# Kernel optimization log

Measured on AMD Instinct MI355X. Metric: run time of the kernel, lower is better.

## Reference

```python
import jax, jax.numpy as jnp
import numpy as np

B, H, S, D = 4, 16, 2048, 64  # head_dim = num_dims // num_heads = 1024 // 16


def setup_inputs() -> dict:
    key = jax.random.key(0)
    kq, kk, kv = jax.random.split(key, 3)
    q = jax.random.normal(kq, (B, H, S, D), dtype=jnp.float32)
    k = jax.random.normal(kk, (B, H, S, D), dtype=jnp.float32)
    v = jax.random.normal(kv, (B, H, S, D), dtype=jnp.float32)
    return {"q": q, "k": k, "v": v}


def reference(q, k, v):
    # scores = (q @ k^T) / sqrt(head_dim)  -> [B, H, S, S]
    scale = 1.0 / np.sqrt(D).astype(np.float32)
    scores = jnp.einsum("bhqd,bhkd->bhqk", q, k) * scale
    # softmax over keys; dropout rate is 0.0 (eval), so it's the identity
    weights = jax.nn.softmax(scores, axis=-1)
    # weights @ v -> [B, H, S, D]
    return jnp.einsum("bhqk,bhkd->bhqd", weights, v)
```

## Files before the change

### kernel.cpp

```cpp
#include <hip/hip_runtime.h>
#include <hip/hip_bf16.h>

#define S_LEN 2048
#define BH_TOTAL 64
#define D_DIM 64
#define NT 32

typedef float f32x4 __attribute__((ext_vector_type(4)));
typedef float f32x16 __attribute__((ext_vector_type(16)));
typedef __bf16 bf16x8 __attribute__((ext_vector_type(8)));
typedef unsigned short u16x8 __attribute__((ext_vector_type(8)));
typedef unsigned int u32;
typedef u32 u32x2 __attribute__((ext_vector_type(2)));
typedef u32 u32x4 __attribute__((ext_vector_type(4)));

union BF8 { u32x4 w; u16x8 u; bf16x8 b; };

#if __has_builtin(__builtin_amdgcn_exp2f)
#define EX2(x) __builtin_amdgcn_exp2f(x)
#else
#define EX2(x) exp2f(x)
#endif

__device__ __forceinline__ unsigned short f2b(float f) {
  __bf16 h = (__bf16)f;
  return __builtin_bit_cast(unsigned short, h);
}
__device__ __forceinline__ u32 pk2(float a, float b) {
  return (u32)f2b(a) | ((u32)f2b(b) << 16);
}

__device__ __forceinline__ u32x2 pl32(u32 x, u32 y) {
#if __has_builtin(__builtin_amdgcn_permlane32_swap)
  return __builtin_amdgcn_permlane32_swap(x, y, false, false);
#else
  u32 xs = (u32)__shfl_xor((int)x, 32);
  u32 ys = (u32)__shfl_xor((int)y, 32);
  int hi = (int)(threadIdx.x & 32);
  u32x2 r;
  r.x = hi ? ys : x;
  r.y = hi ? y : xs;
  return r;
#endif
}

__device__ __forceinline__ void gload16(const unsigned short* g, unsigned short* l) {
  __builtin_amdgcn_global_load_lds(
      (const __attribute__((address_space(1))) unsigned int*)g,
      (__attribute__((address_space(3))) unsigned int*)l, 16, 0, 0);
}

__global__ __launch_bounds__(256)
void cvt_k(const float* __restrict__ K, unsigned short* __restrict__ Kb) {
  int i = blockIdx.x * 256 + threadIdx.x;
  const f32x4* src = (const f32x4*)K;
  f32x4 a = src[2 * i], b = src[2 * i + 1];
  u16x8 o;
  #pragma unroll
  for (int j = 0; j < 4; ++j) { o[j] = f2b(a[j]); o[j + 4] = f2b(b[j]); }
  ((u16x8*)Kb)[i] = o;
}

__global__ __launch_bounds__(256)
void tr_v(const float* __restrict__ V, unsigned short* __restrict__ Vt) {
  __shared__ unsigned short T[64][72];
  int bh = blockIdx.x >> 5, t5 = blockIdx.x & 31;
  int s0 = t5 * 64;
  int tid = threadIdx.x;
  {
    int s = tid >> 2, d0 = (tid & 3) * 16;
    const float* src = V + ((size_t)bh * S_LEN + s0 + s) * D_DIM + d0;
    #pragma unroll
    for (int j = 0; j < 16; j += 4) {
      f32x4 x = *(const f32x4*)(src + j);
      #pragma unroll
      for (int q2 = 0; q2 < 4; ++q2) T[d0 + j + q2][s] = f2b(x[q2]);
    }
  }
  __syncthreads();
  {
    int d = tid >> 2, c0 = (tid & 3) * 16;
    unsigned short* dst = Vt + ((size_t)bh * D_DIM + d) * S_LEN + s0 + c0;
    u16x8 o;
    #pragma unroll
    for (int q2 = 0; q2 < 8; ++q2) o[q2] = T[d][c0 + q2];
    *(u16x8*)dst = o;
    #pragma unroll
    for (int q2 = 0; q2 < 8; ++q2) o[q2] = T[d][c0 + 8 + q2];
    *(u16x8*)(dst + 8) = o;
  }
}

__device__ __forceinline__ void exppack(const f32x16 sv, float& ls, BF8& pA, BF8& pB) {
  u32 wlo[4], whi[4];
  #pragma unroll
  for (int b2 = 0; b2 < 4; ++b2) {
    float e0 = EX2(sv[4 * b2 + 0]), e1 = EX2(sv[4 * b2 + 1]);
    float e2 = EX2(sv[4 * b2 + 2]), e3 = EX2(sv[4 * b2 + 3]);
    ls += (e0 + e1) + (e2 + e3);
    wlo[b2] = pk2(e0, e1);
    whi[b2] = pk2(e2, e3);
  }
  u32x2 rlo = pl32(wlo[0], wlo[1]);
  u32x2 rhi = pl32(whi[0], whi[1]);
  pA.w[0] = rlo.x; pA.w[1] = rhi.x; pA.w[2] = rlo.y; pA.w[3] = rhi.y;
  rlo = pl32(wlo[2], wlo[3]);
  rhi = pl32(whi[2], whi[3]);
  pB.w[0] = rlo.x; pB.w[1] = rhi.x; pB.w[2] = rlo.y; pB.w[3] = rhi.y;
}

#define MFMA32(A, B, C) __builtin_amdgcn_mfma_f32_32x32x16_bf16((A), (B), (C), 0, 0, 0)

__global__ __launch_bounds__(256, 4)
void attn_fwd(const float* __restrict__ Q, const unsigned short* __restrict__ Kb,
              const unsigned short* __restrict__ Vt, float* __restrict__ O) {
  const int wg = blockIdx.x;
  const int id = (wg & 7) * 128 + (wg >> 3);
  const int qt = id & 15;
  const int bh = id >> 4;

  const int tid = threadIdx.x;
  const int w = tid >> 6;
  const int ln = tid & 63;
  const int l31 = ln & 31;
  const int h = ln >> 5;

  __shared__ __align__(16) unsigned short Ks[2][4096];
  __shared__ __align__(16) unsigned short Vs[2][4096];

  const size_t hbase = (size_t)bh * S_LEN * D_DIM;
  const unsigned short* Kh = Kb + hbase;
  const unsigned short* Vh = Vt + hbase;

  const int q0 = qt * 128 + w * 32;

  BF8 qf[4];
  {
    const float sc = 0.125f * 1.44269504088896f;
    const float* qp = Q + hbase + (size_t)(q0 + l31) * D_DIM + h * 8;
    #pragma unroll
    for (int f = 0; f < 4; ++f) {
      f32x4 a = *(const f32x4*)(qp + f * 16);
      f32x4 b = *(const f32x4*)(qp + f * 16 + 4);
      #pragma unroll
      for (int j = 0; j < 4; ++j) {
        qf[f].u[j]     = f2b(a[j] * sc);
        qf[f].u[j + 4] = f2b(b[j] * sc);
      }
    }
  }

  const int srow = ln >> 3;
  const int scol = ((ln & 7) ^ srow) * 8;
  const unsigned short* ks0 = Kh + (size_t)(w * 16 + srow) * D_DIM + scol;
  const unsigned short* vs0 = Vh + (size_t)(w * 16 + srow) * S_LEN + scol;

  const int swz = (ln & 7) << 4;
  const int rb = l31 * 128;
  int cx[4];
  #pragma unroll
  for (int m = 0; m < 4; ++m) cx[m] = (m * 32 + h * 16) ^ swz;

  f32x16 oa0, oa1, zc;
  #pragma unroll
  for (int j = 0; j < 16; ++j) { oa0[j] = 0.f; oa1[j] = 0.f; zc[j] = 0.f; }
  float ls = 0.f;

  gload16(ks0,             &Ks[0][w * 1024]);
  gload16(ks0 + 512,       &Ks[0][w * 1024 + 512]);
  gload16(vs0,             &Vs[0][w * 1024]);
  gload16(vs0 + 8 * S_LEN, &Vs[0][w * 1024 + 512]);
  __syncthreads();

  for (int t = 0; t < NT; ++t) {
    const int cur = t & 1;
    if (t + 1 < NT) {
      const unsigned short* kp = ks0 + (size_t)(t + 1) * 4096;
      const unsigned short* vp = vs0 + (t + 1) * 64;
      gload16(kp,             &Ks[cur ^ 1][w * 1024]);
      gload16(kp + 512,       &Ks[cur ^ 1][w * 1024 + 512]);
      gload16(vp,             &Vs[cur ^ 1][w * 1024]);
      gload16(vp + 8 * S_LEN, &Vs[cur ^ 1][w * 1024 + 512]);
    }

    const char* KsB = (const char*)&Ks[cur][0];
    const char* VsB = (const char*)&Vs[cur][0];

    BF8 ka, kb, kc, kd;
    ka.u = *(const u16x8*)(KsB + rb + cx[0]);
    kb.u = *(const u16x8*)(KsB + 4096 + rb + cx[0]);
    kc.u = *(const u16x8*)(KsB + rb + cx[1]);
    kd.u = *(const u16x8*)(KsB + 4096 + rb + cx[1]);
    f32x16 s0, s1;
    __builtin_amdgcn_s_setprio(1);
    s0 = MFMA32(ka.b, qf[0].b, zc);
    s1 = MFMA32(kb.b, qf[0].b, zc);
    ka.u = *(const u16x8*)(KsB + rb + cx[2]);
    kb.u = *(const u16x8*)(KsB + 4096 + rb + cx[2]);
    s0 = MFMA32(kc.b, qf[1].b, s0);
    s1 = MFMA32(kd.b, qf[1].b, s1);
    kc.u = *(const u16x8*)(KsB + rb + cx[3]);
    kd.u = *(const u16x8*)(KsB + 4096 + rb + cx[3]);
    s0 = MFMA32(ka.b, qf[2].b, s0);
    s1 = MFMA32(kb.b, qf[2].b, s1);
    s0 = MFMA32(kc.b, qf[3].b, s0);
    s1 = MFMA32(kd.b, qf[3].b, s1);
    __builtin_amdgcn_s_setprio(0);

    BF8 va, vb, vc, vd;
    va.u = *(const u16x8*)(VsB + rb + cx[0]);
    vb.u = *(const u16x8*)(VsB + 4096 + rb + cx[0]);
    vc.u = *(const u16x8*)(VsB + rb + cx[1]);
    vd.u = *(const u16x8*)(VsB + 4096 + rb + cx[1]);

    BF8 pf0, pf1, pf2, pf3;
    exppack(s0, ls, pf0, pf1);
    exppack(s1, ls, pf2, pf3);

    __builtin_amdgcn_s_setprio(1);
    oa0 = MFMA32(va.b, pf0.b, oa0);
    oa1 = MFMA32(vb.b, pf0.b, oa1);
    va.u = *(const u16x8*)(VsB + rb + cx[2]);
    vb.u = *(const u16x8*)(VsB + 4096 + rb + cx[2]);
    oa0 = MFMA32(vc.b, pf1.b, oa0);
    oa1 = MFMA32(vd.b, pf1.b, oa1);
    vc.u = *(const u16x8*)(VsB + rb + cx[3]);
    vd.u = *(const u16x8*)(VsB + 4096 + rb + cx[3]);
    oa0 = MFMA32(va.b, pf2.b, oa0);
    oa1 = MFMA32(vb.b, pf2.b, oa1);
    oa0 = MFMA32(vc.b, pf3.b, oa0);
    oa1 = MFMA32(vd.b, pf3.b, oa1);
    __builtin_amdgcn_s_setprio(0);

    __syncthreads();
  }

  {
    float lo2 = __shfl_xor(ls, 32);
    float inv = 1.0f / (ls + lo2);
    float* op = O + hbase + (size_t)(q0 + l31) * D_DIM;
    #pragma unroll
    for (int dt = 0; dt < 2; ++dt) {
      const f32x16 oa = dt ? oa1 : oa0;
      #pragma unroll
      for (int b2 = 0; b2 < 4; ++b2) {
        f32x4 vv;
        vv[0] = oa[4 * b2 + 0] * inv;
        vv[1] = oa[4 * b2 + 1] * inv;
        vv[2] = oa[4 * b2 + 2] * inv;
        vv[3] = oa[4 * b2 + 3] * inv;
        *(f32x4*)(op + dt * 32 + b2 * 8 + h * 4) = vv;
      }
    }
  }
}

extern "C" void kernel_launch(void* const* d_in, const int* in_sizes, int n_in,
                              void* d_out, int out_size, void* d_ws, size_t ws_size,
                              hipStream_t stream) {
  const float* q = (const float*)d_in[0];
  const float* k = (const float*)d_in[1];
  const float* v = (const float*)d_in[2];
  float* o = (float*)d_out;
  unsigned short* kb = (unsigned short*)d_ws;
  unsigned short* vt = kb + (size_t)BH_TOTAL * S_LEN * D_DIM;

  cvt_k<<<dim3(4096), 256, 0, stream>>>(k, kb);
  tr_v<<<dim3(2048), 256, 0, stream>>>(v, vt);
  attn_fwd<<<dim3(1024), 256, 0, stream>>>(q, kb, vt, o);
}
```

Before: 112.3 us.

## Triple-buffer K/V LDS tiles with two-deep prefetch and partial vmcnt waits

Switches the K/V shared-memory staging from double to triple buffering, prefetching two tiles ahead with rotating buffer pointers. The full __syncthreads is replaced by s_waitcnt vmcnt(4) plus s_barrier, so only the older tile's loads must finish before each iteration. This hides more global-load latency, but LDS use rises from 32KB to 48KB per block and the launch-bounds occupancy hint drops from 4 to 3 blocks. The zero accumulators for S are now reinitialised inside the loop.

```diff
diff --git a/kernel.cpp b/kernel.cpp
--- a/kernel.cpp
+++ b/kernel.cpp
@@ -111,7 +111,7 @@
 
 #define MFMA32(A, B, C) __builtin_amdgcn_mfma_f32_32x32x16_bf16((A), (B), (C), 0, 0, 0)
 
-__global__ __launch_bounds__(256, 4)
+__global__ __launch_bounds__(256, 3)
 void attn_fwd(const float* __restrict__ Q, const unsigned short* __restrict__ Kb,
               const unsigned short* __restrict__ Vt, float* __restrict__ O) {
   const int wg = blockIdx.x;
@@ -125,8 +125,8 @@
   const int l31 = ln & 31;
   const int h = ln >> 5;
 
-  __shared__ __align__(16) unsigned short Ks[2][4096];
-  __shared__ __align__(16) unsigned short Vs[2][4096];
+  __shared__ __align__(16) unsigned short Ks[3][4096];
+  __shared__ __align__(16) unsigned short Vs[3][4096];
 
   const size_t hbase = (size_t)bh * S_LEN * D_DIM;
   const unsigned short* Kh = Kb + hbase;
@@ -161,46 +161,56 @@
   #pragma unroll
   for (int m = 0; m < 4; ++m) cx[m] = (m * 32 + h * 16) ^ swz;
 
-  f32x16 oa0, oa1, zc;
-  #pragma unroll
-  for (int j = 0; j < 16; ++j) { oa0[j] = 0.f; oa1[j] = 0.f; zc[j] = 0.f; }
+  f32x16 oa0, oa1;
+  #pragma unroll
+  for (int j = 0; j < 16; ++j) { oa0[j] = 0.f; oa1[j] = 0.f; }
   float ls = 0.f;
 
-  gload16(ks0,             &Ks[0][w * 1024]);
-  gload16(ks0 + 512,       &Ks[0][w * 1024 + 512]);
-  gload16(vs0,             &Vs[0][w * 1024]);
-  gload16(vs0 + 8 * S_LEN, &Vs[0][w * 1024 + 512]);
-  __syncthreads();
+  gload16(ks0,                  &Ks[0][w * 1024]);
+  gload16(ks0 + 512,            &Ks[0][w * 1024 + 512]);
+  gload16(vs0,                  &Vs[0][w * 1024]);
+  gload16(vs0 + 8 * S_LEN,      &Vs[0][w * 1024 + 512]);
+  gload16(ks0 + 4096,           &Ks[1][w * 1024]);
+  gload16(ks0 + 4096 + 512,     &Ks[1][w * 1024 + 512]);
+  gload16(vs0 + 64,             &Vs[1][w * 1024]);
+  gload16(vs0 + 64 + 8 * S_LEN, &Vs[1][w * 1024 + 512]);
+  asm volatile("s_waitcnt vmcnt(4)" ::: "memory");
+  __builtin_amdgcn_s_barrier();
+
+  const char* kA = (const char*)&Ks[0][0];
+  const char* kB = (const char*)&Ks[1][0];
+  char*       kC = (char*)&Ks[2][0];
+  const char* vA = (const char*)&Vs[0][0];
+  const char* vB = (const char*)&Vs[1][0];
+  char*       vC = (char*)&Vs[2][0];
 
   for (int t = 0; t < NT; ++t) {
-    const int cur = t & 1;
-    if (t + 1 < NT) {
-      const unsigned short* kp = ks0 + (size_t)(t + 1) * 4096;
-      const unsigned short* vp = vs0 + (t + 1) * 64;
-      gload16(kp,             &Ks[cur ^ 1][w * 1024]);
-      gload16(kp + 512,       &Ks[cur ^ 1][w * 1024 + 512]);
-      gload16(vp,             &Vs[cur ^ 1][w * 1024]);
-      gload16(vp + 8 * S_LEN, &Vs[cur ^ 1][w * 1024 + 512]);
-    }
-
-    const char* KsB = (const char*)&Ks[cur][0];
-    const char* VsB = (const char*)&Vs[cur][0];
+    if (t + 2 < NT) {
+      const unsigned short* kp = ks0 + (size_t)(t + 2) * 4096;
+      const unsigned short* vp = vs0 + (t + 2) * 64;
+      gload16(kp,             (unsigned short*)kC + w * 1024);
+      gload16(kp + 512,       (unsigned short*)kC + w * 1024 + 512);
+      gload16(vp,             (unsigned short*)vC + w * 1024);
+      gload16(vp + 8 * S_LEN, (unsigned short*)vC + w * 1024 + 512);
+    }
 
     BF8 ka, kb, kc, kd;
-    ka.u = *(const u16x8*)(KsB + rb + cx[0]);
-    kb.u = *(const u16x8*)(KsB + 4096 + rb + cx[0]);
-    kc.u = *(const u16x8*)(KsB + rb + cx[1]);
-    kd.u = *(const u16x8*)(KsB + 4096 + rb + cx[1]);
+    ka.u = *(const u16x8*)(kA + rb + cx[0]);
+    kb.u = *(const u16x8*)(kA + 4096 + rb + cx[0]);
+    kc.u = *(const u16x8*)(kA + rb + cx[1]);
+    kd.u = *(const u16x8*)(kA + 4096 + rb + cx[1]);
     f32x16 s0, s1;
+    #pragma unroll
+    for (int j = 0; j < 16; ++j) { s0[j] = 0.f; s1[j] = 0.f; }
     __builtin_amdgcn_s_setprio(1);
-    s0 = MFMA32(ka.b, qf[0].b, zc);
-    s1 = MFMA32(kb.b, qf[0].b, zc);
-    ka.u = *(const u16x8*)(KsB + rb + cx[2]);
-    kb.u = *(const u16x8*)(KsB + 4096 + rb + cx[2]);
+    s0 = MFMA32(ka.b, qf[0].b, s0);
+    s1 = MFMA32(kb.b, qf[0].b, s1);
+    ka.u = *(const u16x8*)(kA + rb + cx[2]);
+    kb.u = *(const u16x8*)(kA + 4096 + rb + cx[2]);
     s0 = MFMA32(kc.b, qf[1].b, s0);
     s1 = MFMA32(kd.b, qf[1].b, s1);
-    kc.u = *(const u16x8*)(KsB + rb + cx[3]);
-    kd.u = *(const u16x8*)(KsB + 4096 + rb + cx[3]);
+    kc.u = *(const u16x8*)(kA + rb + cx[3]);
+    kd.u = *(const u16x8*)(kA + 4096 + rb + cx[3]);
     s0 = MFMA32(ka.b, qf[2].b, s0);
     s1 = MFMA32(kb.b, qf[2].b, s1);
     s0 = MFMA32(kc.b, qf[3].b, s0);
@@ -208,10 +218,10 @@
     __builtin_amdgcn_s_setprio(0);
 
     BF8 va, vb, vc, vd;
-    va.u = *(const u16x8*)(VsB + rb + cx[0]);
-    vb.u = *(const u16x8*)(VsB + 4096 + rb + cx[0]);
-    vc.u = *(const u16x8*)(VsB + rb + cx[1]);
-    vd.u = *(const u16x8*)(VsB + 4096 + rb + cx[1]);
+    va.u = *(const u16x8*)(vA + rb + cx[0]);
+    vb.u = *(const u16x8*)(vA + 4096 + rb + cx[0]);
+    vc.u = *(const u16x8*)(vA + rb + cx[1]);
+    vd.u = *(const u16x8*)(vA + 4096 + rb + cx[1]);
 
     BF8 pf0, pf1, pf2, pf3;
     exppack(s0, ls, pf0, pf1);
@@ -220,19 +230,27 @@
     __builtin_amdgcn_s_setprio(1);
     oa0 = MFMA32(va.b, pf0.b, oa0);
     oa1 = MFMA32(vb.b, pf0.b, oa1);
-    va.u = *(const u16x8*)(VsB + rb + cx[2]);
-    vb.u = *(const u16x8*)(VsB + 4096 + rb + cx[2]);
+    va.u = *(const u16x8*)(vA + rb + cx[2]);
+    vb.u = *(const u16x8*)(vA + 4096 + rb + cx[2]);
     oa0 = MFMA32(vc.b, pf1.b, oa0);
     oa1 = MFMA32(vd.b, pf1.b, oa1);
-    vc.u = *(const u16x8*)(VsB + rb + cx[3]);
-    vd.u = *(const u16x8*)(VsB + 4096 + rb + cx[3]);
+    vc.u = *(const u16x8*)(vA + rb + cx[3]);
+    vd.u = *(const u16x8*)(vA + 4096 + rb + cx[3]);
     oa0 = MFMA32(va.b, pf2.b, oa0);
     oa1 = MFMA32(vb.b, pf2.b, oa1);
     oa0 = MFMA32(vc.b, pf3.b, oa0);
     oa1 = MFMA32(vd.b, pf3.b, oa1);
     __builtin_amdgcn_s_setprio(0);
 
-    __syncthreads();
+    if (t + 2 < NT) {
+      asm volatile("s_waitcnt vmcnt(4)" ::: "memory");
+    } else {
+      asm volatile("s_waitcnt vmcnt(0)" ::: "memory");
+    }
+    __builtin_amdgcn_s_barrier();
+
+    { const char* tmp = kA; kA = kB; kB = (const char*)kC; kC = (char*)tmp; }
+    { const char* tmp = vA; vA = vB; vB = (const char*)vC; vC = (char*)tmp; }
   }
 
   {
```

Result: slower. 116.0 us (+3.3%).

## Restructure attention K/V pipeline with per-wave full-tile loads and vmcnt waits

Applied to the files above, without the earlier changes.

The attention main loop is rewritten so each wave issues global-to-LDS loads for the whole next K/V tile itself. Synchronisation now uses explicit vmcnt waits plus a raw s_barrier in place of __syncthreads. The score computation is split into two 32-key halves, each followed by its exp/pack and P·V MFMAs, to interleave work and shrink live registers. The K conversion and V transpose prep kernels are merged into one launch. In exchange, every wave fetches the full tile, so global and L2 load traffic is four times larger, and the hand-written wait counts depend on how the compiler orders the loads.

```diff
diff --git a/kernel.cpp b/kernel.cpp
--- a/kernel.cpp
+++ b/kernel.cpp
@@ -51,43 +51,44 @@
 }
 
 __global__ __launch_bounds__(256)
-void cvt_k(const float* __restrict__ K, unsigned short* __restrict__ Kb) {
-  int i = blockIdx.x * 256 + threadIdx.x;
-  const f32x4* src = (const f32x4*)K;
-  f32x4 a = src[2 * i], b = src[2 * i + 1];
-  u16x8 o;
-  #pragma unroll
-  for (int j = 0; j < 4; ++j) { o[j] = f2b(a[j]); o[j + 4] = f2b(b[j]); }
-  ((u16x8*)Kb)[i] = o;
-}
-
-__global__ __launch_bounds__(256)
-void tr_v(const float* __restrict__ V, unsigned short* __restrict__ Vt) {
+void prep(const float* __restrict__ K, const float* __restrict__ V,
+          unsigned short* __restrict__ Kb, unsigned short* __restrict__ Vt) {
   __shared__ unsigned short T[64][72];
-  int bh = blockIdx.x >> 5, t5 = blockIdx.x & 31;
-  int s0 = t5 * 64;
-  int tid = threadIdx.x;
-  {
-    int s = tid >> 2, d0 = (tid & 3) * 16;
-    const float* src = V + ((size_t)bh * S_LEN + s0 + s) * D_DIM + d0;
-    #pragma unroll
-    for (int j = 0; j < 16; j += 4) {
-      f32x4 x = *(const f32x4*)(src + j);
-      #pragma unroll
-      for (int q2 = 0; q2 < 4; ++q2) T[d0 + j + q2][s] = f2b(x[q2]);
-    }
-  }
-  __syncthreads();
-  {
-    int d = tid >> 2, c0 = (tid & 3) * 16;
-    unsigned short* dst = Vt + ((size_t)bh * D_DIM + d) * S_LEN + s0 + c0;
+  if (blockIdx.x < 4096) {
+    int i = blockIdx.x * 256 + threadIdx.x;
+    const f32x4* src = (const f32x4*)K;
+    f32x4 a = src[2 * i], b = src[2 * i + 1];
     u16x8 o;
     #pragma unroll
-    for (int q2 = 0; q2 < 8; ++q2) o[q2] = T[d][c0 + q2];
-    *(u16x8*)dst = o;
-    #pragma unroll
-    for (int q2 = 0; q2 < 8; ++q2) o[q2] = T[d][c0 + 8 + q2];
-    *(u16x8*)(dst + 8) = o;
+    for (int j = 0; j < 4; ++j) { o[j] = f2b(a[j]); o[j + 4] = f2b(b[j]); }
+    ((u16x8*)Kb)[i] = o;
+  } else {
+    int bid = blockIdx.x - 4096;
+    int bh = bid >> 5, t5 = bid & 31;
+    int s0 = t5 * 64;
+    int tid = threadIdx.x;
+    {
+      int s = tid >> 2, d0 = (tid & 3) * 16;
+      const float* src = V + ((size_t)bh * S_LEN + s0 + s) * D_DIM + d0;
+      #pragma unroll
+      for (int j = 0; j < 16; j += 4) {
+        f32x4 x = *(const f32x4*)(src + j);
+        #pragma unroll
+        for (int q2 = 0; q2 < 4; ++q2) T[d0 + j + q2][s] = f2b(x[q2]);
+      }
+    }
+    __syncthreads();
+    {
+      int d = tid >> 2, c0 = (tid & 3) * 16;
+      unsigned short* dst = Vt + ((size_t)bh * D_DIM + d) * S_LEN + s0 + c0;
+      u16x8 o;
+      #pragma unroll
+      for (int q2 = 0; q2 < 8; ++q2) o[q2] = T[d][c0 + q2];
+      *(u16x8*)dst = o;
+      #pragma unroll
+      for (int q2 = 0; q2 < 8; ++q2) o[q2] = T[d][c0 + 8 + q2];
+      *(u16x8*)(dst + 8) = o;
+    }
   }
 }
 
@@ -111,6 +112,67 @@
 
 #define MFMA32(A, B, C) __builtin_amdgcn_mfma_f32_32x32x16_bf16((A), (B), (C), 0, 0, 0)
 
+#define STAGE(tt, SB) do {                                                   \
+    const unsigned short* kp_ = kbase + (size_t)(tt) * 4096;                 \
+    const unsigned short* vp_ = vbase + (tt) * 64;                           \
+    gload16(kp_ + 0 * 512, &Ks[SB][0 * 512]);                                \
+    gload16(kp_ + 1 * 512, &Ks[SB][1 * 512]);                                \
+    gload16(kp_ + 2 * 512, &Ks[SB][2 * 512]);                                \
+    gload16(kp_ + 3 * 512, &Ks[SB][3 * 512]);                                \
+    gload16(kp_ + 4 * 512, &Ks[SB][4 * 512]);                                \
+    gload16(kp_ + 5 * 512, &Ks[SB][5 * 512]);                                \
+    gload16(kp_ + 6 * 512, &Ks[SB][6 * 512]);                                \
+    gload16(kp_ + 7 * 512, &Ks[SB][7 * 512]);                                \
+    gload16(vp_ + (size_t)0 * 8 * S_LEN, &Vs[SB][0 * 512]);                  \
+    gload16(vp_ + (size_t)1 * 8 * S_LEN, &Vs[SB][1 * 512]);                  \
+    gload16(vp_ + (size_t)2 * 8 * S_LEN, &Vs[SB][2 * 512]);                  \
+    gload16(vp_ + (size_t)3 * 8 * S_LEN, &Vs[SB][3 * 512]);                  \
+    gload16(vp_ + (size_t)4 * 8 * S_LEN, &Vs[SB][4 * 512]);                  \
+    gload16(vp_ + (size_t)5 * 8 * S_LEN, &Vs[SB][5 * 512]);                  \
+    gload16(vp_ + (size_t)6 * 8 * S_LEN, &Vs[SB][6 * 512]);                  \
+    gload16(vp_ + (size_t)7 * 8 * S_LEN, &Vs[SB][7 * 512]);                  \
+  } while (0)
+
+#define ITER(tt, RB, SB, DOSTAGE) do {                                       \
+    if (DOSTAGE) { STAGE((tt) + 1, SB); }                                    \
+    const char* KsB_ = (const char*)&Ks[RB][0];                              \
+    const char* VsB_ = (const char*)&Vs[RB][0];                              \
+    _Pragma("unroll")                                                        \
+    for (int kt = 0; kt < 2; ++kt) {                                         \
+      BF8 k0_, k1_, k2_, k3_;                                                \
+      k0_.u = *(const u16x8*)(KsB_ + kt * 4096 + rb + cx[0]);                \
+      k1_.u = *(const u16x8*)(KsB_ + kt * 4096 + rb + cx[1]);                \
+      k2_.u = *(const u16x8*)(KsB_ + kt * 4096 + rb + cx[2]);                \
+      k3_.u = *(const u16x8*)(KsB_ + kt * 4096 + rb + cx[3]);                \
+      f32x16 s_;                                                             \
+      _Pragma("unroll")                                                      \
+      for (int j = 0; j < 16; ++j) s_[j] = 0.f;                              \
+      __builtin_amdgcn_s_setprio(1);                                         \
+      s_ = MFMA32(k0_.b, qf[0].b, s_);                                       \
+      s_ = MFMA32(k1_.b, qf[1].b, s_);                                       \
+      s_ = MFMA32(k2_.b, qf[2].b, s_);                                       \
+      s_ = MFMA32(k3_.b, qf[3].b, s_);                                       \
+      __builtin_amdgcn_s_setprio(0);                                         \
+      BF8 pA_, pB_;                                                          \
+      exppack(s_, ls, pA_, pB_);                                             \
+      if (kt == 0) {                                                         \
+        if (DOSTAGE) asm volatile("s_waitcnt vmcnt(16)" ::: "memory");       \
+        else         asm volatile("s_waitcnt vmcnt(0)"  ::: "memory");       \
+      }                                                                      \
+      BF8 vA0_, vA1_, vB0_, vB1_;                                            \
+      vA0_.u = *(const u16x8*)(VsB_ + rb + cx[2 * kt]);                      \
+      vA1_.u = *(const u16x8*)(VsB_ + 4096 + rb + cx[2 * kt]);               \
+      vB0_.u = *(const u16x8*)(VsB_ + rb + cx[2 * kt + 1]);                  \
+      vB1_.u = *(const u16x8*)(VsB_ + 4096 + rb + cx[2 * kt + 1]);           \
+      __builtin_amdgcn_s_setprio(1);                                         \
+      oa0 = MFMA32(vA0_.b, pA_.b, oa0);                                      \
+      oa1 = MFMA32(vA1_.b, pA_.b, oa1);                                      \
+      oa0 = MFMA32(vB0_.b, pB_.b, oa0);                                      \
+      oa1 = MFMA32(vB1_.b, pB_.b, oa1);                                      \
+      __builtin_amdgcn_s_setprio(0);                                         \
+    }                                                                        \
+  } while (0)
+
 __global__ __launch_bounds__(256, 4)
 void attn_fwd(const float* __restrict__ Q, const unsigned short* __restrict__ Kb,
               const unsigned short* __restrict__ Vt, float* __restrict__ O) {
@@ -152,8 +214,8 @@
 
   const int srow = ln >> 3;
   const int scol = ((ln & 7) ^ srow) * 8;
-  const unsigned short* ks0 = Kh + (size_t)(w * 16 + srow) * D_DIM + scol;
-  const unsigned short* vs0 = Vh + (size_t)(w * 16 + srow) * S_LEN + scol;
+  const unsigned short* kbase = Kh + srow * D_DIM + scol;
+  const unsigned short* vbase = Vh + (size_t)srow * S_LEN + scol;
 
   const int swz = (ln & 7) << 4;
   const int rb = l31 * 128;
@@ -161,79 +223,27 @@
   #pragma unroll
   for (int m = 0; m < 4; ++m) cx[m] = (m * 32 + h * 16) ^ swz;
 
-  f32x16 oa0, oa1, zc;
+  f32x16 oa0, oa1;
   #pragma unroll
-  for (int j = 0; j < 16; ++j) { oa0[j] = 0.f; oa1[j] = 0.f; zc[j] = 0.f; }
+  for (int j = 0; j < 16; ++j) { oa0[j] = 0.f; oa1[j] = 0.f; }
   float ls = 0.f;
 
-  gload16(ks0,             &Ks[0][w * 1024]);
-  gload16(ks0 + 512,       &Ks[0][w * 1024 + 512]);
-  gload16(vs0,             &Vs[0][w * 1024]);
-  gload16(vs0 + 8 * S_LEN, &Vs[0][w * 1024 + 512]);
-  __syncthreads();
-
-  for (int t = 0; t < NT; ++t) {
-    const int cur = t & 1;
-    if (t + 1 < NT) {
-      const unsigned short* kp = ks0 + (size_t)(t + 1) * 4096;
-      const unsigned short* vp = vs0 + (t + 1) * 64;
-      gload16(kp,             &Ks[cur ^ 1][w * 1024]);
-      gload16(kp + 512,       &Ks[cur ^ 1][w * 1024 + 512]);
-      gload16(vp,             &Vs[cur ^ 1][w * 1024]);
-      gload16(vp + 8 * S_LEN, &Vs[cur ^ 1][w * 1024 + 512]);
-    }
-
-    const char* KsB = (const char*)&Ks[cur][0];
-    const char* VsB = (const char*)&Vs[cur][0];
-
-    BF8 ka, kb, kc, kd;
-    ka.u = *(const u16x8*)(KsB + rb + cx[0]);
-    kb.u = *(const u16x8*)(KsB + 4096 + rb + cx[0]);
-    kc.u = *(const u16x8*)(KsB + rb + cx[1]);
-    kd.u = *(const u16x8*)(KsB + 4096 + rb + cx[1]);
-    f32x16 s0, s1;
-    __builtin_amdgcn_s_setprio(1);
-    s0 = MFMA32(ka.b, qf[0].b, zc);
-    s1 = MFMA32(kb.b, qf[0].b, zc);
-    ka.u = *(const u16x8*)(KsB + rb + cx[2]);
-    kb.u = *(const u16x8*)(KsB + 4096 + rb + cx[2]);
-    s0 = MFMA32(kc.b, qf[1].b, s0);
-    s1 = MFMA32(kd.b, qf[1].b, s1);
-    kc.u = *(const u16x8*)(KsB + rb + cx[3]);
-    kd.u = *(const u16x8*)(KsB + 4096 + rb + cx[3]);
-    s0 = MFMA32(ka.b, qf[2].b, s0);
-    s1 = MFMA32(kb.b, qf[2].b, s1);
-    s0 = MFMA32(kc.b, qf[3].b, s0);
-    s1 = MFMA32(kd.b, qf[3].b, s1);
-    __builtin_amdgcn_s_setprio(0);
-
-    BF8 va, vb, vc, vd;
-    va.u = *(const u16x8*)(VsB + rb + cx[0]);
-    vb.u = *(const u16x8*)(VsB + 4096 + rb + cx[0]);
-    vc.u = *(const u16x8*)(VsB + rb + cx[1]);
-    vd.u = *(const u16x8*)(VsB + 4096 + rb + cx[1]);
-
-    BF8 pf0, pf1, pf2, pf3;
-    exppack(s0, ls, pf0, pf1);
-    exppack(s1, ls, pf2, pf3);
-
-    __builtin_amdgcn_s_setprio(1);
-    oa0 = MFMA32(va.b, pf0.b, oa0);
-    oa1 = MFMA32(vb.b, pf0.b, oa1);
-    va.u = *(const u16x8*)(VsB + rb + cx[2]);
-    vb.u = *(const u16x8*)(VsB + 4096 + rb + cx[2]);
-    oa0 = MFMA32(vc.b, pf1.b, oa0);
-    oa1 = MFMA32(vd.b, pf1.b, oa1);
-    vc.u = *(const u16x8*)(VsB + rb + cx[3]);
-    vd.u = *(const u16x8*)(VsB + 4096 + rb + cx[3]);
-    oa0 = MFMA32(va.b, pf2.b, oa0);
-    oa1 = MFMA32(vb.b, pf2.b, oa1);
-    oa0 = MFMA32(vc.b, pf3.b, oa0);
-    oa1 = MFMA32(vd.b, pf3.b, oa1);
-    __builtin_amdgcn_s_setprio(0);
-
-    __syncthreads();
-  }
+  STAGE(0, 0);
+  asm volatile("s_waitcnt vmcnt(8)" ::: "memory");
+  __builtin_amdgcn_s_barrier();
+
+  for (int t2 = 0; t2 < NT - 2; t2 += 2) {
+    ITER(t2, 0, 1, 1);
+    asm volatile("s_waitcnt vmcnt(8)" ::: "memory");
+    __builtin_amdgcn_s_barrier();
+    ITER(t2 + 1, 1, 0, 1);
+    asm volatile("s_waitcnt vmcnt(8)" ::: "memory");
+    __builtin_amdgcn_s_barrier();
+  }
+  ITER(NT - 2, 0, 1, 1);
+  asm volatile("s_waitcnt vmcnt(8)" ::: "memory");
+  __builtin_amdgcn_s_barrier();
+  ITER(NT - 1, 1, 0, 0);
 
   {
     float lo2 = __shfl_xor(ls, 32);
@@ -265,7 +275,6 @@
   unsigned short* kb = (unsigned short*)d_ws;
   unsigned short* vt = kb + (size_t)BH_TOTAL * S_LEN * D_DIM;
 
-  cvt_k<<<dim3(4096), 256, 0, stream>>>(k, kb);
-  tr_v<<<dim3(2048), 256, 0, stream>>>(v, vt);
+  prep<<<dim3(4096 + 2048), 256, 0, stream>>>(k, v, kb, vt);
   attn_fwd<<<dim3(1024), 256, 0, stream>>>(q, kb, vt, o);
 }
```

New measurement: 144.4 us. +28.6%, slower.

## Enlarge attention workgroups to 8 waves with 128-key tiles and fuse prep kernels

Applied to the files above, without the earlier changes.

The attention kernel now uses 512-thread workgroups covering 256 queries. Each loop iteration stages 128 keys as two 64-key chunks, which halves the number of barriers and makes each staged K/V tile serve twice as many queries. The K conversion and V transpose kernels are merged into one launch, saving a kernel launch. The risk is that `__launch_bounds__(512, 4)` implies 8 waves per SIMD, which could cap registers low enough to cause spills given the large MFMA accumulator state.

```diff
diff --git a/kernel.cpp b/kernel.cpp
--- a/kernel.cpp
+++ b/kernel.cpp
@@ -4,7 +4,7 @@
 #define S_LEN 2048
 #define BH_TOTAL 64
 #define D_DIM 64
-#define NT 32
+#define NT2 16
 
 typedef float f32x4 __attribute__((ext_vector_type(4)));
 typedef float f32x16 __attribute__((ext_vector_type(16)));
@@ -51,43 +51,44 @@
 }
 
 __global__ __launch_bounds__(256)
-void cvt_k(const float* __restrict__ K, unsigned short* __restrict__ Kb) {
-  int i = blockIdx.x * 256 + threadIdx.x;
-  const f32x4* src = (const f32x4*)K;
-  f32x4 a = src[2 * i], b = src[2 * i + 1];
-  u16x8 o;
-  #pragma unroll
-  for (int j = 0; j < 4; ++j) { o[j] = f2b(a[j]); o[j + 4] = f2b(b[j]); }
-  ((u16x8*)Kb)[i] = o;
-}
-
-__global__ __launch_bounds__(256)
-void tr_v(const float* __restrict__ V, unsigned short* __restrict__ Vt) {
+void prep(const float* __restrict__ K, const float* __restrict__ V,
+          unsigned short* __restrict__ Kb, unsigned short* __restrict__ Vt) {
   __shared__ unsigned short T[64][72];
-  int bh = blockIdx.x >> 5, t5 = blockIdx.x & 31;
-  int s0 = t5 * 64;
-  int tid = threadIdx.x;
-  {
-    int s = tid >> 2, d0 = (tid & 3) * 16;
-    const float* src = V + ((size_t)bh * S_LEN + s0 + s) * D_DIM + d0;
-    #pragma unroll
-    for (int j = 0; j < 16; j += 4) {
-      f32x4 x = *(const f32x4*)(src + j);
-      #pragma unroll
-      for (int q2 = 0; q2 < 4; ++q2) T[d0 + j + q2][s] = f2b(x[q2]);
-    }
-  }
-  __syncthreads();
-  {
-    int d = tid >> 2, c0 = (tid & 3) * 16;
-    unsigned short* dst = Vt + ((size_t)bh * D_DIM + d) * S_LEN + s0 + c0;
+  if (blockIdx.x < 4096) {
+    int i = blockIdx.x * 256 + threadIdx.x;
+    const f32x4* src = (const f32x4*)K;
+    f32x4 a = src[2 * i], b = src[2 * i + 1];
     u16x8 o;
     #pragma unroll
-    for (int q2 = 0; q2 < 8; ++q2) o[q2] = T[d][c0 + q2];
-    *(u16x8*)dst = o;
-    #pragma unroll
-    for (int q2 = 0; q2 < 8; ++q2) o[q2] = T[d][c0 + 8 + q2];
-    *(u16x8*)(dst + 8) = o;
+    for (int j = 0; j < 4; ++j) { o[j] = f2b(a[j]); o[j + 4] = f2b(b[j]); }
+    ((u16x8*)Kb)[i] = o;
+  } else {
+    int bid = blockIdx.x - 4096;
+    int bh = bid >> 5, t5 = bid & 31;
+    int s0 = t5 * 64;
+    int tid = threadIdx.x;
+    {
+      int s = tid >> 2, d0 = (tid & 3) * 16;
+      const float* src = V + ((size_t)bh * S_LEN + s0 + s) * D_DIM + d0;
+      #pragma unroll
+      for (int j = 0; j < 16; j += 4) {
+        f32x4 x = *(const f32x4*)(src + j);
+        #pragma unroll
+        for (int q2 = 0; q2 < 4; ++q2) T[d0 + j + q2][s] = f2b(x[q2]);
+      }
+    }
+    __syncthreads();
+    {
+      int d = tid >> 2, c0 = (tid & 3) * 16;
+      unsigned short* dst = Vt + ((size_t)bh * D_DIM + d) * S_LEN + s0 + c0;
+      u16x8 o;
+      #pragma unroll
+      for (int q2 = 0; q2 < 8; ++q2) o[q2] = T[d][c0 + q2];
+      *(u16x8*)dst = o;
+      #pragma unroll
+      for (int q2 = 0; q2 < 8; ++q2) o[q2] = T[d][c0 + 8 + q2];
+      *(u16x8*)(dst + 8) = o;
+    }
   }
 }
 
@@ -111,13 +112,13 @@
 
 #define MFMA32(A, B, C) __builtin_amdgcn_mfma_f32_32x32x16_bf16((A), (B), (C), 0, 0, 0)
 
-__global__ __launch_bounds__(256, 4)
+__global__ __launch_bounds__(512, 4)
 void attn_fwd(const float* __restrict__ Q, const unsigned short* __restrict__ Kb,
               const unsigned short* __restrict__ Vt, float* __restrict__ O) {
   const int wg = blockIdx.x;
-  const int id = (wg & 7) * 128 + (wg >> 3);
-  const int qt = id & 15;
-  const int bh = id >> 4;
+  const int id = (wg & 7) * 64 + (wg >> 3);
+  const int qt = id & 7;
+  const int bh = id >> 3;
 
   const int tid = threadIdx.x;
   const int w = tid >> 6;
@@ -125,14 +126,14 @@
   const int l31 = ln & 31;
   const int h = ln >> 5;
 
-  __shared__ __align__(16) unsigned short Ks[2][4096];
-  __shared__ __align__(16) unsigned short Vs[2][4096];
+  __shared__ __align__(16) unsigned short Ks[2][2][4096];
+  __shared__ __align__(16) unsigned short Vs[2][2][4096];
 
   const size_t hbase = (size_t)bh * S_LEN * D_DIM;
   const unsigned short* Kh = Kb + hbase;
   const unsigned short* Vh = Vt + hbase;
 
-  const int q0 = qt * 128 + w * 32;
+  const int q0 = qt * 256 + w * 32;
 
   BF8 qf[4];
   {
@@ -152,8 +153,8 @@
 
   const int srow = ln >> 3;
   const int scol = ((ln & 7) ^ srow) * 8;
-  const unsigned short* ks0 = Kh + (size_t)(w * 16 + srow) * D_DIM + scol;
-  const unsigned short* vs0 = Vh + (size_t)(w * 16 + srow) * S_LEN + scol;
+  const unsigned short* kbase = Kh + (size_t)(w * 8 + srow) * D_DIM + scol;
+  const unsigned short* vbase = Vh + (size_t)(w * 8 + srow) * S_LEN + scol;
 
   const int swz = (ln & 7) << 4;
   const int rb = l31 * 128;
@@ -161,76 +162,72 @@
   #pragma unroll
   for (int m = 0; m < 4; ++m) cx[m] = (m * 32 + h * 16) ^ swz;
 
-  f32x16 oa0, oa1, zc;
+  f32x16 oa0, oa1;
   #pragma unroll
-  for (int j = 0; j < 16; ++j) { oa0[j] = 0.f; oa1[j] = 0.f; zc[j] = 0.f; }
+  for (int j = 0; j < 16; ++j) { oa0[j] = 0.f; oa1[j] = 0.f; }
   float ls = 0.f;
 
-  gload16(ks0,             &Ks[0][w * 1024]);
-  gload16(ks0 + 512,       &Ks[0][w * 1024 + 512]);
-  gload16(vs0,             &Vs[0][w * 1024]);
-  gload16(vs0 + 8 * S_LEN, &Vs[0][w * 1024 + 512]);
+  gload16(kbase,        &Ks[0][0][w * 512]);
+  gload16(kbase + 4096, &Ks[0][1][w * 512]);
+  gload16(vbase,        &Vs[0][0][w * 512]);
+  gload16(vbase + 64,   &Vs[0][1][w * 512]);
   __syncthreads();
 
-  for (int t = 0; t < NT; ++t) {
+  for (int t = 0; t < NT2; ++t) {
     const int cur = t & 1;
-    if (t + 1 < NT) {
-      const unsigned short* kp = ks0 + (size_t)(t + 1) * 4096;
-      const unsigned short* vp = vs0 + (t + 1) * 64;
-      gload16(kp,             &Ks[cur ^ 1][w * 1024]);
-      gload16(kp + 512,       &Ks[cur ^ 1][w * 1024 + 512]);
-      gload16(vp,             &Vs[cur ^ 1][w * 1024]);
-      gload16(vp + 8 * S_LEN, &Vs[cur ^ 1][w * 1024 + 512]);
-    }
-
-    const char* KsB = (const char*)&Ks[cur][0];
-    const char* VsB = (const char*)&Vs[cur][0];
-
-    BF8 ka, kb, kc, kd;
-    ka.u = *(const u16x8*)(KsB + rb + cx[0]);
-    kb.u = *(const u16x8*)(KsB + 4096 + rb + cx[0]);
-    kc.u = *(const u16x8*)(KsB + rb + cx[1]);
-    kd.u = *(const u16x8*)(KsB + 4096 + rb + cx[1]);
-    f32x16 s0, s1;
-    __builtin_amdgcn_s_setprio(1);
-    s0 = MFMA32(ka.b, qf[0].b, zc);
-    s1 = MFMA32(kb.b, qf[0].b, zc);
-    ka.u = *(const u16x8*)(KsB + rb + cx[2]);
-    kb.u = *(const u16x8*)(KsB + 4096 + rb + cx[2]);
-    s0 = MFMA32(kc.b, qf[1].b, s0);
-    s1 = MFMA32(kd.b, qf[1].b, s1);
-    kc.u = *(const u16x8*)(KsB + rb + cx[3]);
-    kd.u = *(const u16x8*)(KsB + 4096 + rb + cx[3]);
-    s0 = MFMA32(ka.b, qf[2].b, s0);
-    s1 = MFMA32(kb.b, qf[2].b, s1);
-    s0 = MFMA32(kc.b, qf[3].b, s0);
-    s1 = MFMA32(kd.b, qf[3].b, s1);
-    __builtin_amdgcn_s_setprio(0);
-
-    BF8 va, vb, vc, vd;
-    va.u = *(const u16x8*)(VsB + rb + cx[0]);
-    vb.u = *(const u16x8*)(VsB + 4096 + rb + cx[0]);
-    vc.u = *(const u16x8*)(VsB + rb + cx[1]);
-    vd.u = *(const u16x8*)(VsB + 4096 + rb + cx[1]);
-
-    BF8 pf0, pf1, pf2, pf3;
-    exppack(s0, ls, pf0, pf1);
-    exppack(s1, ls, pf2, pf3);
-
-    __builtin_amdgcn_s_setprio(1);
-    oa0 = MFMA32(va.b, pf0.b, oa0);
-    oa1 = MFMA32(vb.b, pf0.b, oa1);
-    va.u = *(const u16x8*)(VsB + rb + cx[2]);
-    vb.u = *(const u16x8*)(VsB + 4096 + rb + cx[2]);
-    oa0 = MFMA32(vc.b, pf1.b, oa0);
-    oa1 = MFMA32(vd.b, pf1.b, oa1);
-    vc.u = *(const u16x8*)(VsB + rb + cx[3]);
-    vd.u = *(const u16x8*)(VsB + 4096 + rb + cx[3]);
-    oa0 = MFMA32(va.b, pf2.b, oa0);
-    oa1 = MFMA32(vb.b, pf2.b, oa1);
-    oa0 = MFMA32(vc.b, pf3.b, oa0);
-    oa1 = MFMA32(vd.b, pf3.b, oa1);
-    __builtin_amdgcn_s_setprio(0);
+    if (t + 1 < NT2) {
+      const unsigned short* kp = kbase + (size_t)(t + 1) * 8192;
+      const unsigned short* vp = vbase + (t + 1) * 128;
+      gload16(kp,        &Ks[cur ^ 1][0][w * 512]);
+      gload16(kp + 4096, &Ks[cur ^ 1][1][w * 512]);
+      gload16(vp,        &Vs[cur ^ 1][0][w * 512]);
+      gload16(vp + 64,   &Vs[cur ^ 1][1][w * 512]);
+    }
+
+    #pragma unroll
+    for (int c = 0; c < 2; ++c) {
+      const char* KsB = (const char*)&Ks[cur][c][0];
+      const char* VsB = (const char*)&Vs[cur][c][0];
+
+      f32x16 s0, s1;
+      #pragma unroll
+      for (int j = 0; j < 16; ++j) { s0[j] = 0.f; s1[j] = 0.f; }
+      __builtin_amdgcn_s_setprio(1);
+      #pragma unroll
+      for (int f = 0; f < 4; ++f) {
+        BF8 k0, k1;
+        k0.u = *(const u16x8*)(KsB + rb + cx[f]);
+        k1.u = *(const u16x8*)(KsB + 4096 + rb + cx[f]);
+        s0 = MFMA32(k0.b, qf[f].b, s0);
+        s1 = MFMA32(k1.b, qf[f].b, s1);
+      }
+      __builtin_amdgcn_s_setprio(0);
+
+      BF8 va, vb, vc, vd;
+      va.u = *(const u16x8*)(VsB + rb + cx[0]);
+      vb.u = *(const u16x8*)(VsB + 4096 + rb + cx[0]);
+      vc.u = *(const u16x8*)(VsB + rb + cx[1]);
+      vd.u = *(const u16x8*)(VsB + 4096 + rb + cx[1]);
+
+      BF8 pf0, pf1, pf2, pf3;
+      exppack(s0, ls, pf0, pf1);
+      exppack(s1, ls, pf2, pf3);
+
+      __builtin_amdgcn_s_setprio(1);
+      oa0 = MFMA32(va.b, pf0.b, oa0);
+      oa1 = MFMA32(vb.b, pf0.b, oa1);
+      va.u = *(const u16x8*)(VsB + rb + cx[2]);
+      vb.u = *(const u16x8*)(VsB + 4096 + rb + cx[2]);
+      oa0 = MFMA32(vc.b, pf1.b, oa0);
+      oa1 = MFMA32(vd.b, pf1.b, oa1);
+      vc.u = *(const u16x8*)(VsB + rb + cx[3]);
+      vd.u = *(const u16x8*)(VsB + 4096 + rb + cx[3]);
+      oa0 = MFMA32(va.b, pf2.b, oa0);
+      oa1 = MFMA32(vb.b, pf2.b, oa1);
+      oa0 = MFMA32(vc.b, pf3.b, oa0);
+      oa1 = MFMA32(vd.b, pf3.b, oa1);
+      __builtin_amdgcn_s_setprio(0);
+    }
 
     __syncthreads();
   }
@@ -265,7 +262,6 @@
   unsigned short* kb = (unsigned short*)d_ws;
   unsigned short* vt = kb + (size_t)BH_TOTAL * S_LEN * D_DIM;
 
-  cvt_k<<<dim3(4096), 256, 0, stream>>>(k, kb);
-  tr_v<<<dim3(2048), 256, 0, stream>>>(v, vt);
-  attn_fwd<<<dim3(1024), 256, 0, stream>>>(q, kb, vt, o);
-}
+  prep<<<dim3(4096 + 2048), 256, 0, stream>>>(k, v, kb, vt);
+  attn_fwd<<<dim3(512), 512, 0, stream>>>(q, kb, vt, o);
+}
```

Result: faster. 106.3 us (-5.4%).
